# Optimization experiments

Hardware: AMD Instinct MI355X
Metric: run time of the kernel (lower is better)

Reference implementation:

```python
import jax, jax.numpy as jnp
import numpy as np

N_VOXELS = 262144  # active output voxels (stride=1 -> same coord set as input)


def setup_inputs() -> dict:
    key = jax.random.key(0)
    k1, k2, k3, k4 = jax.random.split(key, 4)
    N, C_IN, C_OUT, K, M = N_VOXELS, 64, 64, 27, 65536
    x = jax.random.normal(k1, (N, C_IN), dtype=jnp.float32)
    W = jax.random.normal(k2, (K, C_IN, C_OUT), dtype=jnp.float32) * (1.0 / np.sqrt(C_IN * K))
    in_map = jax.random.randint(k3, (K, M), 0, N, dtype=jnp.int32)
    out_map = jax.random.randint(k4, (K, M), 0, N, dtype=jnp.int32)
    return {"x": x, "W": W, "in_map": in_map, "out_map": out_map}


def reference(x, W, in_map, out_map):
    # Sparse (Minkowski-style) convolution: gather -> per-offset GEMM -> scatter-add.
    # x: [N, Cin], W: [K, Cin, Cout], in_map/out_map: [K, M] indices into voxel list.
    N = x.shape[0]
    C_out = W.shape[-1]
    gathered = x[in_map]                              # [K, M, Cin]  (irregular gather)
    msg = jnp.einsum('kmc,kcd->kmd', gathered, W)     # [K, M, Cout] per-offset GEMM
    out = jnp.zeros((N, C_out), dtype=x.dtype)
    out = out.at[out_map.reshape(-1)].add(msg.reshape(-1, C_out))  # scatter-add
    return out
```

## Files before the change

### kernel.cpp

```cpp
#include <hip/hip_runtime.h>


typedef __attribute__((ext_vector_type(8))) short bf16x8;
typedef __attribute__((ext_vector_type(8))) unsigned short u16x8;
typedef __attribute__((ext_vector_type(4))) unsigned short u16x4;
typedef __attribute__((ext_vector_type(4))) float f32x4;
typedef __attribute__((ext_vector_type(2))) float f32x2;

constexpr int KOFF = 27;
constexpr int M = 65536;
constexpr int CIN = 64;
constexpr int COUT = 64;
constexpr int NVOX = 262144;
constexpr int NMSG = KOFF * M;
constexpr int TM_BLOCK = 512;
constexpr int TILES_PER_K = M / TM_BLOCK;
constexpr int SUBTILES = TM_BLOCK / (4 * 16);
constexpr int XCVT_BLOCKS = NVOX * CIN / 8 / 256;

static __device__ __forceinline__ short f2bf(float f) {
  unsigned u = __builtin_bit_cast(unsigned, f);
  unsigned r = (u + 0x7FFFu + ((u >> 16) & 1u)) >> 16;
  return (short)r;
}
static __device__ __forceinline__ float bf2f(unsigned short h) {
  return __builtin_bit_cast(float, (unsigned)h << 16);
}

__global__ __launch_bounds__(256) void xw_kernel(
    const float* __restrict__ x, const float* __restrict__ W,
    unsigned short* __restrict__ xb, unsigned short* __restrict__ Wf,
    int xcvtBlocks) {
  const int b = blockIdx.x;
  if (b < xcvtBlocks) {
    int i = b * 256 + threadIdx.x;
    const float4* p = (const float4*)x + (size_t)i * 2;
    float4 a = p[0], q = p[1];
    u16x8 h;
    h[0] = (unsigned short)f2bf(a.x); h[1] = (unsigned short)f2bf(a.y);
    h[2] = (unsigned short)f2bf(a.z); h[3] = (unsigned short)f2bf(a.w);
    h[4] = (unsigned short)f2bf(q.x); h[5] = (unsigned short)f2bf(q.y);
    h[6] = (unsigned short)f2bf(q.z); h[7] = (unsigned short)f2bf(q.w);
    *(u16x8*)(xb + (size_t)i * 8) = h;
  } else {
    int k = b - xcvtBlocks;
    const float* Wk = W + (size_t)k * (CIN * COUT);
    unsigned short* dst = Wf + (size_t)k * 4096;
#pragma unroll
    for (int i = 0; i < 16; ++i) {
      int e = threadIdx.x * 16 + i;
      int j = e & 7, l = (e >> 3) & 63, tu = e >> 9;
      int t = tu >> 1, u = tu & 1;
      dst[e] = (unsigned short)f2bf(Wk[(u * 32 + (l >> 4) * 8 + j) * COUT + t * 16 + (l & 15)]);
    }
  }
}

__global__ __launch_bounds__(256) void rank_kernel(const int* __restrict__ out_map,
                                                   int* __restrict__ cnt,
                                                   int* __restrict__ rank) {
  int i = (blockIdx.x * 256 + threadIdx.x) * 4;
  int4 om = *(const int4*)(out_map + i);
  int4 rk;
  rk.x = atomicAdd(&cnt[om.x], 1);
  rk.y = atomicAdd(&cnt[om.y], 1);
  rk.z = atomicAdd(&cnt[om.z], 1);
  rk.w = atomicAdd(&cnt[om.w], 1);
  *(int4*)(rank + i) = rk;
}

__global__ __launch_bounds__(256) void scan1_kernel(const int* __restrict__ cnt,
                                                    int* __restrict__ starts,
                                                    int* __restrict__ blockSums) {
  __shared__ int s[256];
  int t = threadIdx.x, i = blockIdx.x * 256 + t;
  int c = cnt[i];
  s[t] = c; __syncthreads();
  for (int off = 1; off < 256; off <<= 1) {
    int add = (t >= off) ? s[t - off] : 0;
    __syncthreads(); s[t] += add; __syncthreads();
  }
  starts[i] = s[t] - c;
  if (t == 255) blockSums[blockIdx.x] = s[t];
}

__global__ __launch_bounds__(256) void scan2_kernel(int* __restrict__ bs) {
  __shared__ int s[256];
  int t = threadIdx.x;
  int v0 = bs[t*4], v1 = bs[t*4+1], v2 = bs[t*4+2], v3 = bs[t*4+3];
  int sum = v0 + v1 + v2 + v3;
  s[t] = sum; __syncthreads();
  for (int off = 1; off < 256; off <<= 1) {
    int add = (t >= off) ? s[t - off] : 0;
    __syncthreads(); s[t] += add; __syncthreads();
  }
  int run = s[t] - sum;
  bs[t*4] = run; run += v0;
  bs[t*4+1] = run; run += v1;
  bs[t*4+2] = run; run += v2;
  bs[t*4+3] = run;
}

__global__ __launch_bounds__(256) void scan3_kernel(int* __restrict__ starts,
                                                    const int* __restrict__ blockBase) {
  int i = blockIdx.x * 256 + threadIdx.x;
  starts[i] += blockBase[blockIdx.x];
  if (i == 0) starts[NVOX] = NMSG;
}

template <bool BF16IN>
__global__ __launch_bounds__(256) void gemm_msg_kernel(
    const void* __restrict__ xin, const unsigned short* __restrict__ Wf,
    const int* __restrict__ in_map, const int* __restrict__ out_map,
    const int* __restrict__ rank, const int* __restrict__ starts,
    unsigned short* __restrict__ msg) {
  const int k = blockIdx.x / TILES_PER_K;
  const int mblock = (blockIdx.x % TILES_PER_K) * TM_BLOCK;
  const int wave = threadIdx.x >> 6;
  const int l = threadIdx.x & 63;
  const int lg = l >> 4;
  const int lr = l & 15;

  bf16x8 bfrag[4][2];
  const bf16x8* wf = (const bf16x8*)(Wf + (size_t)k * 4096);
#pragma unroll
  for (int t = 0; t < 4; ++t)
#pragma unroll
    for (int u = 0; u < 2; ++u)
      bfrag[t][u] = wf[(t * 2 + u) * 64 + l];

  const int mwave = mblock + wave * (TM_BLOCK / 4);
  const int rb = k * M + mwave;

  auto loadA = [&](int s, bf16x8& A0, bf16x8& A1) {
    int id = in_map[rb + s * 16 + lr];
    if (BF16IN) {
      const unsigned short* xr = (const unsigned short*)xin + (size_t)id * CIN + lg * 8;
      A0 = *(const bf16x8*)(xr);
      A1 = *(const bf16x8*)(xr + 32);
    } else {
      const float* xr = (const float*)xin + (size_t)id * CIN + lg * 8;
      float4 x0 = *(const float4*)(xr);
      float4 x1 = *(const float4*)(xr + 4);
      float4 x2 = *(const float4*)(xr + 32);
      float4 x3 = *(const float4*)(xr + 36);
      A0[0]=f2bf(x0.x); A0[1]=f2bf(x0.y); A0[2]=f2bf(x0.z); A0[3]=f2bf(x0.w);
      A0[4]=f2bf(x1.x); A0[5]=f2bf(x1.y); A0[6]=f2bf(x1.z); A0[7]=f2bf(x1.w);
      A1[0]=f2bf(x2.x); A1[1]=f2bf(x2.y); A1[2]=f2bf(x2.z); A1[3]=f2bf(x2.w);
      A1[4]=f2bf(x3.x); A1[5]=f2bf(x3.y); A1[6]=f2bf(x3.z); A1[7]=f2bf(x3.w);
    }
  };

  int om[4], rk[4];
#pragma unroll
  for (int r = 0; r < 4; ++r) {
    om[r] = out_map[rb + lg * 4 + r];
    rk[r] = rank[rb + lg * 4 + r];
  }

  bf16x8 c0, c1, n0, n1;
  loadA(0, c0, c1);
  loadA(1, n0, n1);

#pragma unroll 1
  for (int s = 0; s < SUBTILES; ++s) {
    bf16x8 p0, p1;
    const bool have = (s + 2 < SUBTILES);
    if (have) loadA(s + 2, p0, p1);

    int omN[4], rkN[4];
    if (s + 1 < SUBTILES) {
      const int rowb = rb + (s + 1) * 16 + lg * 4;
#pragma unroll
      for (int r = 0; r < 4; ++r) { omN[r] = out_map[rowb + r]; rkN[r] = rank[rowb + r]; }
    } else {
#pragma unroll
      for (int r = 0; r < 4; ++r) { omN[r] = 0; rkN[r] = 0; }
    }
    int st[4];
#pragma unroll
    for (int r = 0; r < 4; ++r) st[r] = starts[om[r]];

    f32x4 acc[4] = {{0.f,0.f,0.f,0.f},{0.f,0.f,0.f,0.f},{0.f,0.f,0.f,0.f},{0.f,0.f,0.f,0.f}};
#pragma unroll
    for (int t = 0; t < 4; ++t) {
      acc[t] = __builtin_amdgcn_mfma_f32_16x16x32_bf16(c0, bfrag[t][0], acc[t], 0, 0, 0);
      acc[t] = __builtin_amdgcn_mfma_f32_16x16x32_bf16(c1, bfrag[t][1], acc[t], 0, 0, 0);
    }

#pragma unroll
    for (int r = 0; r < 4; ++r) {
      const int sl = st[r] + rk[r];
      u16x4 h;
      h[0] = (unsigned short)f2bf(acc[0][r]);
      h[1] = (unsigned short)f2bf(acc[1][r]);
      h[2] = (unsigned short)f2bf(acc[2][r]);
      h[3] = (unsigned short)f2bf(acc[3][r]);
      __builtin_nontemporal_store(h, (u16x4*)(msg + (size_t)sl * 64 + lr * 4));
    }

    c0 = n0; c1 = n1;
    if (have) { n0 = p0; n1 = p1; }
#pragma unroll
    for (int r = 0; r < 4; ++r) { om[r] = omN[r]; rk[r] = rkN[r]; }
  }
}

__global__ __launch_bounds__(256) void gather_out_kernel(
    const unsigned short* __restrict__ msg, const int* __restrict__ starts,
    float* __restrict__ out) {
  const int wid = (blockIdx.x * 256 + threadIdx.x) >> 6;
  const int p = threadIdx.x & 63;
  const int r = p >> 3;
  const int c = p & 7;
  const int o = wid * 8 + r;

  const int base = starts[o];
  const int n = starts[o + 1] - base;
  const unsigned short* src = msg + (size_t)base * 64 + c * 8;

  u16x8 v[8];
#pragma unroll
  for (int i = 0; i < 8; ++i) {
    int safe = (i < n) ? i : 0;
    v[i] = __builtin_nontemporal_load((const u16x8*)(src + (size_t)safe * 64));
  }
  float acc[8] = {};
#pragma unroll
  for (int i = 0; i < 8; ++i) {
    float m = (i < n) ? 1.0f : 0.0f;
#pragma unroll
    for (int d = 0; d < 8; ++d)
      acc[d] = fmaf(m, bf2f((unsigned short)v[i][d]), acc[d]);
  }
  for (int i = 8; i < n; ++i) {
    u16x8 t = __builtin_nontemporal_load((const u16x8*)(src + (size_t)i * 64));
#pragma unroll
    for (int d = 0; d < 8; ++d) acc[d] += bf2f((unsigned short)t[d]);
  }

  float* orow = out + (size_t)o * 64 + 2 * c;
  f32x2 s0 = {acc[0], acc[4]};
  f32x2 s1 = {acc[1], acc[5]};
  f32x2 s2 = {acc[2], acc[6]};
  f32x2 s3 = {acc[3], acc[7]};
  __builtin_nontemporal_store(s0, (f32x2*)(orow));
  __builtin_nontemporal_store(s1, (f32x2*)(orow + 16));
  __builtin_nontemporal_store(s2, (f32x2*)(orow + 32));
  __builtin_nontemporal_store(s3, (f32x2*)(orow + 48));
}

__global__ __launch_bounds__(256) void spconv_atomic_kernel(
    const float* __restrict__ x, const float* __restrict__ W,
    const int* __restrict__ in_map, const int* __restrict__ out_map,
    float* __restrict__ out) {
  const int k = blockIdx.x / TILES_PER_K;
  const int mblock = (blockIdx.x % TILES_PER_K) * TM_BLOCK;
  const int wave = threadIdx.x >> 6;
  const int l = threadIdx.x & 63;
  const int lg = l >> 4;
  const int lr = l & 15;
  bf16x8 bfrag[4][2];
  const float* Wk = W + (size_t)k * (CIN * COUT);
#pragma unroll
  for (int t = 0; t < 4; ++t)
#pragma unroll
    for (int u = 0; u < 2; ++u)
#pragma unroll
      for (int j = 0; j < 8; ++j)
        bfrag[t][u][j] = f2bf(Wk[(u * 32 + lg * 8 + j) * COUT + t * 16 + lr]);
  const int mwave = mblock + wave * (TM_BLOCK / 4);
#pragma unroll 1
  for (int s = 0; s < SUBTILES; ++s) {
    const int mbase = mwave + s * 16;
    const int in_idx = in_map[k * M + mbase + lr];
    const float* xr = x + (size_t)in_idx * CIN + lg * 8;
    float4 x0 = *(const float4*)(xr);
    float4 x1 = *(const float4*)(xr + 4);
    float4 x2 = *(const float4*)(xr + 32);
    float4 x3 = *(const float4*)(xr + 36);
    bf16x8 a0, a1;
    a0[0]=f2bf(x0.x); a0[1]=f2bf(x0.y); a0[2]=f2bf(x0.z); a0[3]=f2bf(x0.w);
    a0[4]=f2bf(x1.x); a0[5]=f2bf(x1.y); a0[6]=f2bf(x1.z); a0[7]=f2bf(x1.w);
    a1[0]=f2bf(x2.x); a1[1]=f2bf(x2.y); a1[2]=f2bf(x2.z); a1[3]=f2bf(x2.w);
    a1[4]=f2bf(x3.x); a1[5]=f2bf(x3.y); a1[6]=f2bf(x3.z); a1[7]=f2bf(x3.w);
    f32x4 acc[4] = {{0.f,0.f,0.f,0.f},{0.f,0.f,0.f,0.f},{0.f,0.f,0.f,0.f},{0.f,0.f,0.f,0.f}};
#pragma unroll
    for (int t = 0; t < 4; ++t) {
      acc[t] = __builtin_amdgcn_mfma_f32_16x16x32_bf16(a0, bfrag[t][0], acc[t], 0, 0, 0);
      acc[t] = __builtin_amdgcn_mfma_f32_16x16x32_bf16(a1, bfrag[t][1], acc[t], 0, 0, 0);
    }
    const int obase = k * M + mbase + lg * 4;
    int oidx[4];
#pragma unroll
    for (int r = 0; r < 4; ++r) oidx[r] = out_map[obase + r];
#pragma unroll
    for (int t = 0; t < 4; ++t)
#pragma unroll
      for (int r = 0; r < 4; ++r)
        atomicAdd(out + (size_t)oidx[r] * COUT + t * 16 + lr, acc[t][r]);
  }
}

extern "C" void kernel_launch(void* const* d_in, const int* in_sizes, int n_in,
                              void* d_out, int out_size, void* d_ws, size_t ws_size,
                              hipStream_t stream) {
  const float* x = (const float*)d_in[0];
  const float* W = (const float*)d_in[1];
  const int* in_map = (const int*)d_in[2];
  const int* out_map = (const int*)d_in[3];
  float* out = (float*)d_out;
  char* ws = (char*)d_ws;

  const size_t msg_b    = (size_t)NMSG * 128;
  const size_t xb_b     = (size_t)NVOX * CIN * 2;
  const size_t rank_b   = (size_t)NMSG * 4;
  const size_t wf_b     = (size_t)KOFF * 4096 * 2;
  const size_t starts_b = (size_t)(NVOX + 1) * 4;
  const size_t cnt_b    = (size_t)NVOX * 4;
  auto pad = [](size_t b) { return (b + 255) & ~(size_t)255; };

  size_t need_p1 = pad(msg_b) + pad(rank_b) + pad(wf_b) + pad(starts_b);
  size_t need_p0 = need_p1 + pad(xb_b);
  bool useXb = (ws_size >= need_p0);
  bool outScratchOk = ((size_t)out_size * 4 >= cnt_b + 1024 * 4 + 256);

  if (ws_size < need_p1 || !outScratchOk) {
    hipMemsetAsync(d_out, 0, (size_t)out_size * sizeof(float), stream);
    spconv_atomic_kernel<<<dim3(KOFF * TILES_PER_K), dim3(256), 0, stream>>>(
        x, W, in_map, out_map, out);
    return;
  }

  size_t off = 0;
  unsigned short* msg = (unsigned short*)(ws + off); off += pad(msg_b);
  unsigned short* xb = nullptr;
  if (useXb) { xb = (unsigned short*)(ws + off); off += pad(xb_b); }
  int* rank = (int*)(ws + off); off += pad(rank_b);
  unsigned short* Wf = (unsigned short*)(ws + off); off += pad(wf_b);
  int* starts = (int*)(ws + off); off += pad(starts_b);

  int* cnt  = (int*)d_out;
  int* bsum = (int*)d_out + NVOX;

  hipMemsetAsync(cnt, 0, cnt_b, stream);

  int xcvtBlocks = useXb ? XCVT_BLOCKS : 0;
  xw_kernel<<<dim3(xcvtBlocks + KOFF), dim3(256), 0, stream>>>(x, W, xb, Wf, xcvtBlocks);

  rank_kernel<<<dim3(NMSG / 1024), dim3(256), 0, stream>>>(out_map, cnt, rank);

  scan1_kernel<<<dim3(NVOX / 256), dim3(256), 0, stream>>>(cnt, starts, bsum);
  scan2_kernel<<<dim3(1), dim3(256), 0, stream>>>(bsum);
  scan3_kernel<<<dim3(NVOX / 256), dim3(256), 0, stream>>>(starts, bsum);

  if (useXb)
    gemm_msg_kernel<true><<<dim3(KOFF * TILES_PER_K), dim3(256), 0, stream>>>(
        (const void*)xb, Wf, in_map, out_map, rank, starts, msg);
  else
    gemm_msg_kernel<false><<<dim3(KOFF * TILES_PER_K), dim3(256), 0, stream>>>(
        (const void*)x, Wf, in_map, out_map, rank, starts, msg);

  gather_out_kernel<<<dim3(NVOX / 32), dim3(256), 0, stream>>>(msg, starts, out);
}
```

Measured before the change: 228.1 us.

## Drop bf16 x pre-conversion; double per-thread work in rank and gather kernels

Removes the separate x-to-bf16 conversion pass and has the GEMM gather fp32 rows directly, converting them in registers. This drops one full read and write of x plus a pass, but doubles the bytes gathered per message row. The rank kernel now handles 8 entries per thread and the gather-out kernel 2 output voxels per row group. Both are meant to raise memory-level parallelism and cut block counts, at the cost of higher register use.

```diff
diff --git a/kernel.cpp b/kernel.cpp
--- a/kernel.cpp
+++ b/kernel.cpp
@@ -16,7 +16,6 @@
 constexpr int TM_BLOCK = 512;
 constexpr int TILES_PER_K = M / TM_BLOCK;
 constexpr int SUBTILES = TM_BLOCK / (4 * 16);
-constexpr int XCVT_BLOCKS = NVOX * CIN / 8 / 256;
 
 static __device__ __forceinline__ short f2bf(float f) {
   unsigned u = __builtin_bit_cast(unsigned, f);
@@ -27,47 +26,41 @@
   return __builtin_bit_cast(float, (unsigned)h << 16);
 }
 
-__global__ __launch_bounds__(256) void xw_kernel(
-    const float* __restrict__ x, const float* __restrict__ W,
-    unsigned short* __restrict__ xb, unsigned short* __restrict__ Wf,
-    int xcvtBlocks) {
-  const int b = blockIdx.x;
-  if (b < xcvtBlocks) {
-    int i = b * 256 + threadIdx.x;
-    const float4* p = (const float4*)x + (size_t)i * 2;
-    float4 a = p[0], q = p[1];
-    u16x8 h;
-    h[0] = (unsigned short)f2bf(a.x); h[1] = (unsigned short)f2bf(a.y);
-    h[2] = (unsigned short)f2bf(a.z); h[3] = (unsigned short)f2bf(a.w);
-    h[4] = (unsigned short)f2bf(q.x); h[5] = (unsigned short)f2bf(q.y);
-    h[6] = (unsigned short)f2bf(q.z); h[7] = (unsigned short)f2bf(q.w);
-    *(u16x8*)(xb + (size_t)i * 8) = h;
-  } else {
-    int k = b - xcvtBlocks;
-    const float* Wk = W + (size_t)k * (CIN * COUT);
-    unsigned short* dst = Wf + (size_t)k * 4096;
-#pragma unroll
-    for (int i = 0; i < 16; ++i) {
-      int e = threadIdx.x * 16 + i;
-      int j = e & 7, l = (e >> 3) & 63, tu = e >> 9;
-      int t = tu >> 1, u = tu & 1;
-      dst[e] = (unsigned short)f2bf(Wk[(u * 32 + (l >> 4) * 8 + j) * COUT + t * 16 + (l & 15)]);
-    }
-  }
-}
+
+__global__ __launch_bounds__(256) void wf_kernel(const float* __restrict__ W,
+                                                 unsigned short* __restrict__ Wf) {
+  int k = blockIdx.x;
+  const float* Wk = W + (size_t)k * (CIN * COUT);
+  unsigned short* dst = Wf + (size_t)k * 4096;
+#pragma unroll
+  for (int i = 0; i < 16; ++i) {
+    int e = threadIdx.x * 16 + i;
+    int j = e & 7, l = (e >> 3) & 63, tu = e >> 9;
+    int t = tu >> 1, u = tu & 1;
+    dst[e] = (unsigned short)f2bf(Wk[(u * 32 + (l >> 4) * 8 + j) * COUT + t * 16 + (l & 15)]);
+  }
+}
+
 
 __global__ __launch_bounds__(256) void rank_kernel(const int* __restrict__ out_map,
                                                    int* __restrict__ cnt,
                                                    int* __restrict__ rank) {
-  int i = (blockIdx.x * 256 + threadIdx.x) * 4;
-  int4 om = *(const int4*)(out_map + i);
-  int4 rk;
-  rk.x = atomicAdd(&cnt[om.x], 1);
-  rk.y = atomicAdd(&cnt[om.y], 1);
-  rk.z = atomicAdd(&cnt[om.z], 1);
-  rk.w = atomicAdd(&cnt[om.w], 1);
-  *(int4*)(rank + i) = rk;
-}
+  int i = (blockIdx.x * 256 + threadIdx.x) * 8;
+  int4 a = *(const int4*)(out_map + i);
+  int4 b = *(const int4*)(out_map + i + 4);
+  int4 ra, rb;
+  ra.x = atomicAdd(&cnt[a.x], 1);
+  ra.y = atomicAdd(&cnt[a.y], 1);
+  ra.z = atomicAdd(&cnt[a.z], 1);
+  ra.w = atomicAdd(&cnt[a.w], 1);
+  rb.x = atomicAdd(&cnt[b.x], 1);
+  rb.y = atomicAdd(&cnt[b.y], 1);
+  rb.z = atomicAdd(&cnt[b.z], 1);
+  rb.w = atomicAdd(&cnt[b.w], 1);
+  *(int4*)(rank + i) = ra;
+  *(int4*)(rank + i + 4) = rb;
+}
+
 
 __global__ __launch_bounds__(256) void scan1_kernel(const int* __restrict__ cnt,
                                                     int* __restrict__ starts,
@@ -108,9 +101,9 @@
   if (i == 0) starts[NVOX] = NMSG;
 }
 
-template <bool BF16IN>
+
 __global__ __launch_bounds__(256) void gemm_msg_kernel(
-    const void* __restrict__ xin, const unsigned short* __restrict__ Wf,
+    const float* __restrict__ x, const unsigned short* __restrict__ Wf,
     const int* __restrict__ in_map, const int* __restrict__ out_map,
     const int* __restrict__ rank, const int* __restrict__ starts,
     unsigned short* __restrict__ msg) {
@@ -134,21 +127,15 @@
 
   auto loadA = [&](int s, bf16x8& A0, bf16x8& A1) {
     int id = in_map[rb + s * 16 + lr];
-    if (BF16IN) {
-      const unsigned short* xr = (const unsigned short*)xin + (size_t)id * CIN + lg * 8;
-      A0 = *(const bf16x8*)(xr);
-      A1 = *(const bf16x8*)(xr + 32);
-    } else {
-      const float* xr = (const float*)xin + (size_t)id * CIN + lg * 8;
-      float4 x0 = *(const float4*)(xr);
-      float4 x1 = *(const float4*)(xr + 4);
-      float4 x2 = *(const float4*)(xr + 32);
-      float4 x3 = *(const float4*)(xr + 36);
-      A0[0]=f2bf(x0.x); A0[1]=f2bf(x0.y); A0[2]=f2bf(x0.z); A0[3]=f2bf(x0.w);
-      A0[4]=f2bf(x1.x); A0[5]=f2bf(x1.y); A0[6]=f2bf(x1.z); A0[7]=f2bf(x1.w);
-      A1[0]=f2bf(x2.x); A1[1]=f2bf(x2.y); A1[2]=f2bf(x2.z); A1[3]=f2bf(x2.w);
-      A1[4]=f2bf(x3.x); A1[5]=f2bf(x3.y); A1[6]=f2bf(x3.z); A1[7]=f2bf(x3.w);
-    }
+    const float* xr = x + (size_t)id * CIN + lg * 8;
+    float4 x0 = *(const float4*)(xr);
+    float4 x1 = *(const float4*)(xr + 4);
+    float4 x2 = *(const float4*)(xr + 32);
+    float4 x3 = *(const float4*)(xr + 36);
+    A0[0]=f2bf(x0.x); A0[1]=f2bf(x0.y); A0[2]=f2bf(x0.z); A0[3]=f2bf(x0.w);
+    A0[4]=f2bf(x1.x); A0[5]=f2bf(x1.y); A0[6]=f2bf(x1.z); A0[7]=f2bf(x1.w);
+    A1[0]=f2bf(x2.x); A1[1]=f2bf(x2.y); A1[2]=f2bf(x2.z); A1[3]=f2bf(x2.w);
+    A1[4]=f2bf(x3.x); A1[5]=f2bf(x3.y); A1[6]=f2bf(x3.z); A1[7]=f2bf(x3.w);
   };
 
   int om[4], rk[4];
@@ -206,6 +193,7 @@
   }
 }
 
+
 __global__ __launch_bounds__(256) void gather_out_kernel(
     const unsigned short* __restrict__ msg, const int* __restrict__ starts,
     float* __restrict__ out) {
@@ -213,42 +201,66 @@
   const int p = threadIdx.x & 63;
   const int r = p >> 3;
   const int c = p & 7;
-  const int o = wid * 8 + r;
-
-  const int base = starts[o];
-  const int n = starts[o + 1] - base;
-  const unsigned short* src = msg + (size_t)base * 64 + c * 8;
-
-  u16x8 v[8];
+  const int oA = wid * 16 + r;
+  const int oB = oA + 8;
+
+  const int baseA = starts[oA];
+  const int nA = starts[oA + 1] - baseA;
+  const int baseB = starts[oB];
+  const int nB = starts[oB + 1] - baseB;
+  const unsigned short* srcA = msg + (size_t)baseA * 64 + c * 8;
+  const unsigned short* srcB = msg + (size_t)baseB * 64 + c * 8;
+
+  u16x8 vA[8], vB[8];
 #pragma unroll
   for (int i = 0; i < 8; ++i) {
-    int safe = (i < n) ? i : 0;
-    v[i] = __builtin_nontemporal_load((const u16x8*)(src + (size_t)safe * 64));
-  }
-  float acc[8] = {};
+    int sa = (i < nA) ? i : 0;
+    vA[i] = __builtin_nontemporal_load((const u16x8*)(srcA + (size_t)sa * 64));
+  }
 #pragma unroll
   for (int i = 0; i < 8; ++i) {
-    float m = (i < n) ? 1.0f : 0.0f;
-#pragma unroll
-    for (int d = 0; d < 8; ++d)
-      acc[d] = fmaf(m, bf2f((unsigned short)v[i][d]), acc[d]);
-  }
-  for (int i = 8; i < n; ++i) {
-    u16x8 t = __builtin_nontemporal_load((const u16x8*)(src + (size_t)i * 64));
-#pragma unroll
-    for (int d = 0; d < 8; ++d) acc[d] += bf2f((unsigned short)t[d]);
-  }
-
-  float* orow = out + (size_t)o * 64 + 2 * c;
-  f32x2 s0 = {acc[0], acc[4]};
-  f32x2 s1 = {acc[1], acc[5]};
-  f32x2 s2 = {acc[2], acc[6]};
-  f32x2 s3 = {acc[3], acc[7]};
-  __builtin_nontemporal_store(s0, (f32x2*)(orow));
-  __builtin_nontemporal_store(s1, (f32x2*)(orow + 16));
-  __builtin_nontemporal_store(s2, (f32x2*)(orow + 32));
-  __builtin_nontemporal_store(s3, (f32x2*)(orow + 48));
-}
+    int sb = (i < nB) ? i : 0;
+    vB[i] = __builtin_nontemporal_load((const u16x8*)(srcB + (size_t)sb * 64));
+  }
+
+  float accA[8] = {}, accB[8] = {};
+#pragma unroll
+  for (int i = 0; i < 8; ++i) {
+    float mA = (i < nA) ? 1.0f : 0.0f;
+    float mB = (i < nB) ? 1.0f : 0.0f;
+#pragma unroll
+    for (int d = 0; d < 8; ++d) {
+      accA[d] = fmaf(mA, bf2f((unsigned short)vA[i][d]), accA[d]);
+      accB[d] = fmaf(mB, bf2f((unsigned short)vB[i][d]), accB[d]);
+    }
+  }
+  for (int i = 8; i < nA; ++i) {
+    u16x8 t = __builtin_nontemporal_load((const u16x8*)(srcA + (size_t)i * 64));
+#pragma unroll
+    for (int d = 0; d < 8; ++d) accA[d] += bf2f((unsigned short)t[d]);
+  }
+  for (int i = 8; i < nB; ++i) {
+    u16x8 t = __builtin_nontemporal_load((const u16x8*)(srcB + (size_t)i * 64));
+#pragma unroll
+    for (int d = 0; d < 8; ++d) accB[d] += bf2f((unsigned short)t[d]);
+  }
+
+  float* orA = out + (size_t)oA * 64 + 2 * c;
+  float* orB = out + (size_t)oB * 64 + 2 * c;
+  f32x2 a0 = {accA[0], accA[4]}; f32x2 a1 = {accA[1], accA[5]};
+  f32x2 a2 = {accA[2], accA[6]}; f32x2 a3 = {accA[3], accA[7]};
+  f32x2 b0 = {accB[0], accB[4]}; f32x2 b1 = {accB[1], accB[5]};
+  f32x2 b2 = {accB[2], accB[6]}; f32x2 b3 = {accB[3], accB[7]};
+  __builtin_nontemporal_store(a0, (f32x2*)(orA));
+  __builtin_nontemporal_store(a1, (f32x2*)(orA + 16));
+  __builtin_nontemporal_store(a2, (f32x2*)(orA + 32));
+  __builtin_nontemporal_store(a3, (f32x2*)(orA + 48));
+  __builtin_nontemporal_store(b0, (f32x2*)(orB));
+  __builtin_nontemporal_store(b1, (f32x2*)(orB + 16));
+  __builtin_nontemporal_store(b2, (f32x2*)(orB + 32));
+  __builtin_nontemporal_store(b3, (f32x2*)(orB + 48));
+}
+
 
 __global__ __launch_bounds__(256) void spconv_atomic_kernel(
     const float* __restrict__ x, const float* __restrict__ W,
@@ -313,19 +325,16 @@
   char* ws = (char*)d_ws;
 
   const size_t msg_b    = (size_t)NMSG * 128;
-  const size_t xb_b     = (size_t)NVOX * CIN * 2;
   const size_t rank_b   = (size_t)NMSG * 4;
   const size_t wf_b     = (size_t)KOFF * 4096 * 2;
   const size_t starts_b = (size_t)(NVOX + 1) * 4;
   const size_t cnt_b    = (size_t)NVOX * 4;
   auto pad = [](size_t b) { return (b + 255) & ~(size_t)255; };
 
-  size_t need_p1 = pad(msg_b) + pad(rank_b) + pad(wf_b) + pad(starts_b);
-  size_t need_p0 = need_p1 + pad(xb_b);
-  bool useXb = (ws_size >= need_p0);
+  size_t need = pad(msg_b) + pad(rank_b) + pad(wf_b) + pad(starts_b);
   bool outScratchOk = ((size_t)out_size * 4 >= cnt_b + 1024 * 4 + 256);
 
-  if (ws_size < need_p1 || !outScratchOk) {
+  if (ws_size < need || !outScratchOk) {
     hipMemsetAsync(d_out, 0, (size_t)out_size * sizeof(float), stream);
     spconv_atomic_kernel<<<dim3(KOFF * TILES_PER_K), dim3(256), 0, stream>>>(
         x, W, in_map, out_map, out);
@@ -334,8 +343,6 @@
 
   size_t off = 0;
   unsigned short* msg = (unsigned short*)(ws + off); off += pad(msg_b);
-  unsigned short* xb = nullptr;
-  if (useXb) { xb = (unsigned short*)(ws + off); off += pad(xb_b); }
   int* rank = (int*)(ws + off); off += pad(rank_b);
   unsigned short* Wf = (unsigned short*)(ws + off); off += pad(wf_b);
   int* starts = (int*)(ws + off); off += pad(starts_b);
@@ -345,21 +352,15 @@
 
   hipMemsetAsync(cnt, 0, cnt_b, stream);
 
-  int xcvtBlocks = useXb ? XCVT_BLOCKS : 0;
-  xw_kernel<<<dim3(xcvtBlocks + KOFF), dim3(256), 0, stream>>>(x, W, xb, Wf, xcvtBlocks);
-
-  rank_kernel<<<dim3(NMSG / 1024), dim3(256), 0, stream>>>(out_map, cnt, rank);
+  wf_kernel<<<dim3(KOFF), dim3(256), 0, stream>>>(W, Wf);
+  rank_kernel<<<dim3(NMSG / 2048), dim3(256), 0, stream>>>(out_map, cnt, rank);
 
   scan1_kernel<<<dim3(NVOX / 256), dim3(256), 0, stream>>>(cnt, starts, bsum);
   scan2_kernel<<<dim3(1), dim3(256), 0, stream>>>(bsum);
   scan3_kernel<<<dim3(NVOX / 256), dim3(256), 0, stream>>>(starts, bsum);
 
-  if (useXb)
-    gemm_msg_kernel<true><<<dim3(KOFF * TILES_PER_K), dim3(256), 0, stream>>>(
-        (const void*)xb, Wf, in_map, out_map, rank, starts, msg);
-  else
-    gemm_msg_kernel<false><<<dim3(KOFF * TILES_PER_K), dim3(256), 0, stream>>>(
-        (const void*)x, Wf, in_map, out_map, rank, starts, msg);
-
-  gather_out_kernel<<<dim3(NVOX / 32), dim3(256), 0, stream>>>(msg, starts, out);
-}
+  gemm_msg_kernel<<<dim3(KOFF * TILES_PER_K), dim3(256), 0, stream>>>(
+      x, Wf, in_map, out_map, rank, starts, msg);
+
+  gather_out_kernel<<<dim3(NVOX / 64), dim3(256), 0, stream>>>(msg, starts, out);
+}
```

After: 260.1 us. 14.0% more time.
